# Kernel optimization log

Measured on AMD Instinct MI355X. Metric: run time of the kernel, lower is better.

## Reference

```python
import jax, jax.numpy as jnp
import numpy as np

EPS = 1e-6

def rms_norm(x):
    # RMSNorm, affine=False
    return x * jax.lax.rsqrt(jnp.mean(x * x, axis=-1, keepdims=True) + EPS)

def apply_rope(x, cos, sin):
    # x: [N, T, h, d], cos/sin: [T, d//2], half-split rotation
    x1, x2 = jnp.split(x, 2, axis=-1)
    c = cos[None, :, None, :]
    s = sin[None, :, None, :]
    return jnp.concatenate([x1 * c - x2 * s, x1 * s + x2 * c], axis=-1)

def setup_inputs() -> dict:
    key = jax.random.key(0)
    k0, k1, k2 = jax.random.split(key, 3)
    N, T, D, hd = 1, 2048, 2048, 128
    input_NTD = jax.random.normal(k0, (N, T, D), jnp.float32)
    qkv_weight = jax.random.normal(k1, (3, D, D), jnp.float32) / np.sqrt(D) / 2.0
    o_weight = jax.random.normal(k2, (D, D), jnp.float32) * 0.02
    # standard 1d RoPE angle table
    pos = jnp.arange(T, dtype=jnp.float32)
    inv_freq = 1.0 / (10000.0 ** (jnp.arange(hd // 2, dtype=jnp.float32) / (hd // 2)))
    ang = pos[:, None] * inv_freq[None, :]  # [T, hd//2]
    return {
        "input_NTD": input_NTD,
        "qkv_weight": qkv_weight,
        "o_weight": o_weight,
        "cos": jnp.cos(ang),
        "sin": jnp.sin(ang),
    }

def reference(input_NTD, qkv_weight, o_weight, cos, sin):
    N, T, D = input_NTD.shape
    hd = cos.shape[-1] * 2
    h = D // hd
    w = qkv_weight.reshape(3 * D, D)
    qkv = rms_norm(input_NTD) @ w.T                      # [N, T, 3D]
    qkv = qkv.reshape(N, T, 3 * h, hd)
    q, k, v = jnp.split(qkv, 3, axis=2)                  # each [N, T, h, hd]
    q = apply_rope(rms_norm(q), cos, sin)
    k = apply_rope(rms_norm(k), cos, sin)
    scale = 1.0 / np.sqrt(hd)
    scores = jnp.einsum('nqhd,nkhd->nhqk', q, k) * scale  # [N, h, T, T]
    causal = jnp.tril(jnp.ones((T, T), bool))
    scores = jnp.where(causal[None, None], scores, -jnp.inf)
    att = jax.nn.softmax(scores, axis=-1)
    x = jnp.einsum('nhqk,nkhd->nqhd', att, v).reshape(N, T, D)
    out = input_NTD + x @ o_weight.T
    return out, k, v
```

## Files before the change

kernel.cpp:

```cpp
#include <hip/hip_runtime.h>
#include <hip/hip_bf16.h>

typedef unsigned short u16;
typedef unsigned int u32;
typedef __bf16 bf16x8 __attribute__((ext_vector_type(8)));
typedef u16 u16x8 __attribute__((ext_vector_type(8)));
typedef u16 u16x4 __attribute__((ext_vector_type(4)));
typedef float f32x4 __attribute__((ext_vector_type(4)));

#define T_SEQ 2048
#define DMODEL 2048
#define NHEAD 16
#define HDIM 128
#define ATT_SCALE_L2E 0.12751744f

__device__ __forceinline__ u16 f2bf(float f) {
    return __builtin_bit_cast(u16, __float2bfloat16(f));
}
__device__ __forceinline__ bf16x8 as_bf(u16x8 v) {
    return __builtin_bit_cast(bf16x8, v);
}
__device__ __forceinline__ float lo2f(u32 w) { return __builtin_bit_cast(float, w << 16); }
__device__ __forceinline__ float hi2f(u32 w) { return __builtin_bit_cast(float, w & 0xffff0000u); }
__device__ __forceinline__ void gload_lds16(const u16* g, u16* l) {
    __builtin_amdgcn_global_load_lds(
        (const __attribute__((address_space(1))) u32*)(g),
        (__attribute__((address_space(3))) u32*)(l), 16, 0, 0);
}

__global__ __launch_bounds__(256) void cast_both(const float* __restrict__ w1,
                                                 const float* __restrict__ w2,
                                                 u16* __restrict__ d1,
                                                 u16* __restrict__ d2) {
    int i = blockIdx.x * 256 + threadIdx.x;
    const float* src; u16* dst; int k;
    if (i < 1572864) { src = w1; dst = d1; k = i; }
    else             { src = w2; dst = d2; k = i - 1572864; }
    float4 a = ((const float4*)src)[2 * k];
    float4 b = ((const float4*)src)[2 * k + 1];
    u16x8 o;
    o[0] = f2bf(a.x); o[1] = f2bf(a.y); o[2] = f2bf(a.z); o[3] = f2bf(a.w);
    o[4] = f2bf(b.x); o[5] = f2bf(b.y); o[6] = f2bf(b.z); o[7] = f2bf(b.w);
    *(u16x8*)(dst + (size_t)k * 8) = o;
}

__global__ __launch_bounds__(256) void rmsnorm_row(const float* __restrict__ x,
                                                   u16* __restrict__ xn) {
    const int row = blockIdx.x, tid = threadIdx.x;
    const float* xr = x + (size_t)row * DMODEL;
    float4 a = ((const float4*)xr)[2 * tid];
    float4 b = ((const float4*)xr)[2 * tid + 1];
    float ss = a.x*a.x + a.y*a.y + a.z*a.z + a.w*a.w
             + b.x*b.x + b.y*b.y + b.z*b.z + b.w*b.w;
#pragma unroll
    for (int off = 32; off; off >>= 1) ss += __shfl_xor(ss, off);
    __shared__ float red[4];
    if ((tid & 63) == 0) red[tid >> 6] = ss;
    __syncthreads();
    float tot = red[0] + red[1] + red[2] + red[3];
    float r = rsqrtf(tot * (1.f / DMODEL) + 1e-6f);
    u16x8 o;
    o[0] = f2bf(a.x*r); o[1] = f2bf(a.y*r); o[2] = f2bf(a.z*r); o[3] = f2bf(a.w*r);
    o[4] = f2bf(b.x*r); o[5] = f2bf(b.y*r); o[6] = f2bf(b.z*r); o[7] = f2bf(b.w*r);
    *(u16x8*)(xn + (size_t)row * DMODEL + tid * 8) = o;
}

#define VM2 asm volatile("s_waitcnt vmcnt(2)" ::: "memory");
#define VM4 asm volatile("s_waitcnt vmcnt(4)" ::: "memory");
#define VM0 asm volatile("s_waitcnt vmcnt(0)" ::: "memory");

#define ENDP                                                                  \
  __builtin_amdgcn_s_barrier();                                               \
  __builtin_amdgcn_sched_barrier(0);

#define LDA192(BUF, MH)                                                       \
  _Pragma("unroll") for (int mq = 0; mq < 4; ++mq) {                          \
    int ra = wr + (MH) * 64 + mq * 16 + fr;                                   \
    int sw = ra & 7;                                                          \
    _Pragma("unroll") for (int k2 = 0; k2 < 2; ++k2)                          \
      av[mq][k2] = *(const u16x8*)(sA[BUF] + ra * 64 +                        \
                                   ((((k2 << 2) | fg) ^ sw) << 3));           \
  }

#define LDB0_192(BUF)                                                         \
  _Pragma("unroll") for (int nq = 0; nq < 2; ++nq) {                          \
    int rb = wc + nq * 16 + fr;                                               \
    int sw = rb & 7;                                                          \
    _Pragma("unroll") for (int k2 = 0; k2 < 2; ++k2)                          \
      bv[nq][k2] = *(const u16x8*)(sB[BUF] + rb * 64 +                        \
                                   ((((k2 << 2) | fg) ^ sw) << 3));           \
  }

#define LDB1_192(BUF)                                                         \
  {                                                                           \
    int rb = wc + 32 + fr;                                                    \
    int sw = rb & 7;                                                          \
    _Pragma("unroll") for (int k2 = 0; k2 < 2; ++k2)                          \
      bv1[k2] = *(const u16x8*)(sB[BUF] + rb * 64 +                           \
                                ((((k2 << 2) | fg) ^ sw) << 3));              \
  }

#define MFMAQ_N0(MH)                                                          \
  __builtin_amdgcn_s_barrier();                                               \
  __builtin_amdgcn_s_setprio(1);                                              \
  _Pragma("unroll") for (int k2 = 0; k2 < 2; ++k2)                            \
    _Pragma("unroll") for (int mq = 0; mq < 4; ++mq)                          \
      _Pragma("unroll") for (int nq = 0; nq < 2; ++nq)                        \
        acc[(MH) * 4 + mq][nq] = __builtin_amdgcn_mfma_f32_16x16x32_bf16(     \
            as_bf(av[mq][k2]), as_bf(bv[nq][k2]), acc[(MH) * 4 + mq][nq],     \
            0, 0, 0);                                                         \
  __builtin_amdgcn_s_setprio(0);

#define MFMAQ_N1(MH)                                                          \
  __builtin_amdgcn_s_barrier();                                               \
  __builtin_amdgcn_s_setprio(1);                                              \
  _Pragma("unroll") for (int k2 = 0; k2 < 2; ++k2)                            \
    _Pragma("unroll") for (int mq = 0; mq < 4; ++mq)                          \
      acc[(MH) * 4 + mq][2] = __builtin_amdgcn_mfma_f32_16x16x32_bf16(        \
          as_bf(av[mq][k2]), as_bf(bv1[k2]), acc[(MH) * 4 + mq][2],           \
          0, 0, 0);                                                           \
  __builtin_amdgcn_s_setprio(0);

__global__ __launch_bounds__(512) void gemm192(const u16* __restrict__ A,
                                               const u16* __restrict__ B,
                                               u16* __restrict__ C,
                                               int M, int N, int K) {
    extern __shared__ char smem[];
    const int tid = threadIdx.x, lane = tid & 63, wid = tid >> 6;
    const int bm = blockIdx.y * 256, bn = blockIdx.x * 192;
    const int wr = (wid >> 2) * 128, wc = (wid & 3) * 48;
    const int fr = lane & 15, fg = lane >> 4;

    u16* sA[2] = {(u16*)smem, (u16*)(smem + 57344)};
    u16* sB[2] = {(u16*)(smem + 32768), (u16*)(smem + 90112)};

    const int cs = (((tid & 7) ^ ((tid >> 3) & 7)) << 3);
    const int s8 = (tid & 7) << 3;
    const int rr6 = tid >> 3;

    auto stA = [&](int buf, int k0, int mh) {
#pragma unroll
        for (int j = 0; j < 2; ++j) {
            int r = j * 128 + mh * 64 + rr6;
            gload_lds16(A + (size_t)(bm + r) * K + k0 + cs, sA[buf] + r * 64 + s8);
        }
    };
    auto stB = [&](int buf, int k0, int bt) {
        int r = bt * 64 + rr6;
        gload_lds16(B + (size_t)(bn + r) * K + k0 + cs, sB[buf] + r * 64 + s8);
    };

    f32x4 acc[8][3] = {};
    u16x8 av[4][2], bv[2][2], bv1[2];
    const int nt = K >> 6;

    stA(0, 0, 0); stA(0, 0, 1); stB(0, 0, 0); stB(0, 0, 1); stB(0, 0, 2);
    stA(1, 64, 0);
    VM2
    __builtin_amdgcn_s_barrier();
    __builtin_amdgcn_sched_barrier(0);

    for (int it = 0; it < (nt >> 1); ++it) {
        const int kc = it << 7;
        const int kn1 = kc + 64, kn2 = kc + 128, kn3 = kc + 192;
        const bool st2 = (kn2 < K), st3 = (kn3 < K);

        LDA192(0, 0) LDB0_192(0)
        stA(1, kn1, 1); stB(1, kn1, 0);
        MFMAQ_N0(0) ENDP
        LDB1_192(0)
        stB(1, kn1, 1); stB(1, kn1, 2);
        MFMAQ_N1(0) ENDP
        LDA192(0, 1)
        if (st2) stA(0, kn2, 0);
        MFMAQ_N1(1) ENDP
        LDB0_192(0)
        MFMAQ_N0(1)
        if (st2) { VM2 } else { VM0 }
        ENDP
        LDA192(1, 0) LDB0_192(1)
        if (st2) { stA(0, kn2, 1); stB(0, kn2, 0); }
        MFMAQ_N0(0) ENDP
        LDB1_192(1)
        if (st2) { stB(0, kn2, 1); stB(0, kn2, 2); }
        MFMAQ_N1(0) ENDP
        LDA192(1, 1)
        if (st3) stA(1, kn3, 0);
        MFMAQ_N1(1) ENDP
        LDB0_192(1)
        MFMAQ_N0(1)
        if (st3) { VM2 } else { VM0 }
        ENDP
    }

#pragma unroll
    for (int am = 0; am < 8; ++am)
#pragma unroll
        for (int bq = 0; bq < 3; ++bq)
#pragma unroll
            for (int r = 0; r < 4; ++r) {
                int row = bm + wr + am * 16 + fg * 4 + r;
                int col = bn + wc + bq * 16 + fr;
                C[(size_t)row * N + col] = f2bf(acc[am][bq][r]);
            }
}

#define LDAH(BUF, MH)                                                         \
  _Pragma("unroll") for (int mq = 0; mq < 2; ++mq) {                          \
    int ra = wr + (MH) * 32 + mq * 16 + fr;                                   \
    int sw = ra & 7;                                                          \
    _Pragma("unroll") for (int k2 = 0; k2 < 2; ++k2)                          \
      av[mq][k2] = *(const u16x8*)(sA[BUF] + ra * 64 +                        \
                                   ((((k2 << 2) | fg) ^ sw) << 3));           \
  }

#define LDBH(BUF, NH)                                                         \
  _Pragma("unroll") for (int nq = 0; nq < 2; ++nq) {                          \
    int rb = wc + (NH) * 32 + nq * 16 + fr;                                   \
    int sw = rb & 7;                                                          \
    _Pragma("unroll") for (int k2 = 0; k2 < 2; ++k2)                          \
      bv[nq][k2] = *(const u16x8*)(sB[BUF] + rb * 64 +                        \
                                   ((((k2 << 2) | fg) ^ sw) << 3));           \
  }

#define MFMAQH(MH, NH)                                                        \
  __builtin_amdgcn_s_barrier();                                               \
  __builtin_amdgcn_s_setprio(1);                                              \
  _Pragma("unroll") for (int k2 = 0; k2 < 2; ++k2)                            \
    _Pragma("unroll") for (int mq = 0; mq < 2; ++mq)                          \
      _Pragma("unroll") for (int nq = 0; nq < 2; ++nq)                        \
        acc[(MH) * 2 + mq][(NH) * 2 + nq] =                                   \
            __builtin_amdgcn_mfma_f32_16x16x32_bf16(                          \
                as_bf(av[mq][k2]), as_bf(bv[nq][k2]),                         \
                acc[(MH) * 2 + mq][(NH) * 2 + nq], 0, 0, 0);                  \
  __builtin_amdgcn_s_setprio(0);

__global__ __launch_bounds__(256) void gemm128(const u16* __restrict__ A,
                                               const u16* __restrict__ B,
                                               float* __restrict__ C,
                                               const float* __restrict__ resid,
                                               int M, int N, int K) {
    extern __shared__ char smem[];
    const int tid = threadIdx.x, lane = tid & 63, wid = tid >> 6;
    const int bm = blockIdx.y * 128, bn = blockIdx.x * 128;
    const int wr = (wid >> 1) * 64, wc = (wid & 1) * 64;
    const int fr = lane & 15, fg = lane >> 4;

    u16* sA[2] = {(u16*)smem, (u16*)(smem + 32768)};
    u16* sB[2] = {(u16*)(smem + 16384), (u16*)(smem + 49152)};

    const int cs = (((tid & 7) ^ ((tid >> 3) & 7)) << 3);
    const int s8 = (tid & 7) << 3;
    const int rr5 = tid >> 3;

    auto stA = [&](int buf, int k0, int mh) {
#pragma unroll
        for (int j = 0; j < 2; ++j) {
            int r = j * 64 + mh * 32 + rr5;
            gload_lds16(A + (size_t)(bm + r) * K + k0 + cs, sA[buf] + r * 64 + s8);
        }
    };
    auto stB = [&](int buf, int k0, int nh) {
#pragma unroll
        for (int j = 0; j < 2; ++j) {
            int r = j * 64 + nh * 32 + rr5;
            gload_lds16(B + (size_t)(bn + r) * K + k0 + cs, sB[buf] + r * 64 + s8);
        }
    };

    f32x4 acc[4][4] = {};
    u16x8 av[2][2], bv[2][2];
    const int nt = K >> 6;

    stA(0, 0, 0); stA(0, 0, 1); stB(0, 0, 0); stB(0, 0, 1);
    stA(1, 64, 0); stB(1, 64, 1);
    VM4
    __builtin_amdgcn_s_barrier();
    __builtin_amdgcn_sched_barrier(0);

    for (int it = 0; it < (nt >> 1); ++it) {
        const int kc = it << 7;
        const int kn1 = kc + 64, kn2 = kc + 128, kn3 = kc + 192;
        const bool st2 = (kn2 < K), st3 = (kn3 < K);

        LDAH(0, 0) LDBH(0, 0)
        stA(1, kn1, 1);
        MFMAQH(0, 0) ENDP
        LDBH(0, 1)
        stB(1, kn1, 0);
        MFMAQH(0, 1) ENDP
        LDAH(0, 1)
        if (st2) stA(0, kn2, 0);
        MFMAQH(1, 1) ENDP
        LDBH(0, 0)
        if (st2) stB(0, kn2, 1);
        MFMAQH(1, 0)
        if (st2) { VM4 } else { VM0 }
        ENDP
        LDAH(1, 0) LDBH(1, 0)
        if (st2) stA(0, kn2, 1);
        MFMAQH(0, 0) ENDP
        LDBH(1, 1)
        if (st2) stB(0, kn2, 0);
        MFMAQH(0, 1) ENDP
        LDAH(1, 1)
        if (st3) stA(1, kn3, 0);
        MFMAQH(1, 1) ENDP
        LDBH(1, 0)
        if (st3) stB(1, kn3, 1);
        MFMAQH(1, 0)
        VM4
        ENDP
    }

#pragma unroll
    for (int am = 0; am < 4; ++am)
#pragma unroll
        for (int bq = 0; bq < 4; ++bq)
#pragma unroll
            for (int r = 0; r < 4; ++r) {
                int row = bm + wr + am * 16 + fg * 4 + r;
                int col = bn + wc + bq * 16 + fr;
                float val = acc[am][bq][r] + resid[(size_t)row * N + col];
                C[(size_t)row * N + col] = val;
            }
}

__global__ __launch_bounds__(256) void rope_split(const u16* __restrict__ qkv,
                                                  const float* __restrict__ cosb,
                                                  const float* __restrict__ sinb,
                                                  u16* __restrict__ q_bf,
                                                  u16* __restrict__ k_bf,
                                                  float* __restrict__ k_out,
                                                  float* __restrict__ v_out) {
    const int t = blockIdx.x, tid = threadIdx.x, wid = tid >> 6, lane = tid & 63;
    const u16* row = qkv + (size_t)t * (3 * DMODEL);
    const int dp = (lane & 31) << 1;
    float2 c2 = *(const float2*)(cosb + t * 64 + dp);
    float2 s2 = *(const float2*)(sinb + t * 64 + dp);
    const bool hi = lane >= 32;

    for (int task = wid; task < 32; task += 4) {
        u32 w = *(const u32*)(row + task * 128 + lane * 2);
        float xa = lo2f(w), xb = hi2f(w);
        float ss = xa * xa + xb * xb;
#pragma unroll
        for (int off = 32; off; off >>= 1) ss += __shfl_xor(ss, off);
        float rn = rsqrtf(ss * (1.f / 128.f) + 1e-6f);
        float pa = __shfl_xor(xa, 32), pb = __shfl_xor(xb, 32);
        float oa, ob;
        if (!hi) {
            oa = (xa * c2.x - pa * s2.x) * rn;
            ob = (xb * c2.y - pb * s2.y) * rn;
        } else {
            oa = (pa * s2.x + xa * c2.x) * rn;
            ob = (pb * s2.y + xb * c2.y) * rn;
        }
        u32 pk = (u32)f2bf(oa) | ((u32)f2bf(ob) << 16);
        if (task < 16) {
            *(u32*)(q_bf + ((size_t)task * T_SEQ + t) * 128 + lane * 2) = pk;
        } else {
            int hh = task - 16;
            *(u32*)(k_bf + ((size_t)hh * T_SEQ + t) * 128 + lane * 2) = pk;
            float2 kk; kk.x = oa; kk.y = ob;
            *(float2*)(k_out + (size_t)t * DMODEL + hh * 128 + lane * 2) = kk;
        }
    }
    {
        u16x8 vv = *(const u16x8*)(row + 2 * DMODEL + tid * 8);
        float4 f0, f1;
        f0.x = __builtin_bit_cast(float, (u32)vv[0] << 16);
        f0.y = __builtin_bit_cast(float, (u32)vv[1] << 16);
        f0.z = __builtin_bit_cast(float, (u32)vv[2] << 16);
        f0.w = __builtin_bit_cast(float, (u32)vv[3] << 16);
        f1.x = __builtin_bit_cast(float, (u32)vv[4] << 16);
        f1.y = __builtin_bit_cast(float, (u32)vv[5] << 16);
        f1.z = __builtin_bit_cast(float, (u32)vv[6] << 16);
        f1.w = __builtin_bit_cast(float, (u32)vv[7] << 16);
        *(float4*)(v_out + (size_t)t * DMODEL + tid * 8) = f0;
        *(float4*)(v_out + (size_t)t * DMODEL + tid * 8 + 4) = f1;
    }
}

__global__ __launch_bounds__(256) void vtrans(const u16* __restrict__ qkv,
                                              u16* __restrict__ vt) {
    const int b = blockIdx.x, tid = threadIdx.x;
    const int head = b >> 7;
    const int i = (b & 127) * 256 + tid;
    const int d = i & 127, tc = i >> 7;
    u16x8 o;
#pragma unroll
    for (int j = 0; j < 8; ++j)
        o[j] = qkv[(size_t)(tc * 8 + j) * (3 * DMODEL) + 2 * DMODEL + head * 128 + d];
    *(u16x8*)&vt[((size_t)head * 128 + d) * T_SEQ + tc * 8] = o;
}

__global__ __launch_bounds__(256) void attn_fwd(const u16* __restrict__ qb,
                                                const u16* __restrict__ kb,
                                                const u16* __restrict__ vtb,
                                                u16* __restrict__ xout) {
    __shared__ u16 Ks[2][64 * 128];
    __shared__ u16 Vs[2][128 * 64];
    __shared__ u16 Ps[4][16 * 64];

    const int bid = blockIdx.x;
    const int r8 = bid & 7, s = bid >> 3;
    const int head = r8 + ((s >> 5) << 3);
    const int j = s & 31;
    const int qt = (s < 32) ? (31 - j) : j;

    const int tid = threadIdx.x, wid = tid >> 6, lane = tid & 63;
    const int fr = lane & 15, fg = lane >> 4;
    const u16* kh = kb + (size_t)head * T_SEQ * 128;
    const u16* vth = vtb + (size_t)head * 128 * T_SEQ;
    const u16* qh = qb + (size_t)head * T_SEQ * 128;
    const int q0 = qt * 64 + wid * 16;
    const int qrow_g = q0 + fr;

    u16x8 bq[4];
    {
        const u16* qrow = qh + (size_t)(q0 + fr) * 128 + fg * 8;
#pragma unroll
        for (int cc = 0; cc < 4; ++cc) bq[cc] = *(const u16x8*)(qrow + cc * 32);
    }

    auto stage = [&](int kv0, int buf) {
#pragma unroll
        for (int i = 0; i < 4; ++i) {
            int idx = i * 256 + tid;
            int r = idx >> 4;
            int cbs = ((idx & 15) << 4) ^ ((r & 7) << 4);
            gload_lds16(kh + (size_t)(kv0 + r) * 128 + (cbs >> 1), &Ks[buf][idx * 8]);
        }
#pragma unroll
        for (int i = 0; i < 4; ++i) {
            int idx = i * 256 + tid;
            int d = idx >> 3;
            int cbs = ((idx & 7) << 4) ^ ((d & 7) << 4);
            gload_lds16(vth + (size_t)d * T_SEQ + kv0 + (cbs >> 1), &Vs[buf][idx * 8]);
        }
    };

    stage(0, 0);

    f32x4 o[8] = {};
    float m_run = -1e30f, l_run = 0.f;
    const int nt = qt + 1;

    for (int kt = 0; kt < nt; ++kt) {
        const int kv0 = kt * 64;
        const int buf = kt & 1;
        if (kt + 1 < nt) {
            stage(kv0 + 64, buf ^ 1);
            asm volatile("s_waitcnt vmcnt(8)" ::: "memory");
        } else {
            asm volatile("s_waitcnt vmcnt(0)" ::: "memory");
        }
        __builtin_amdgcn_s_barrier();
        __builtin_amdgcn_sched_barrier(0);

        const char* ksb = (const char*)&Ks[buf][0];
        const char* vsb = (const char*)&Vs[buf][0];
        char* psb = (char*)&Ps[wid][0];

        float p[4][4];
        float mx = -1e30f;
        const bool diag = (kv0 + 64 > q0);
#pragma unroll
        for (int st = 0; st < 4; ++st) {
            f32x4 sacc = {0.f, 0.f, 0.f, 0.f};
#pragma unroll
            for (int c4 = 0; c4 < 4; ++c4) {
                int r = st * 16 + fr;
                int cb = c4 * 64 + fg * 16;
                u16x8 ak = *(const u16x8*)(ksb + r * 256 + (cb ^ ((r & 7) << 4)));
                sacc = __builtin_amdgcn_mfma_f32_16x16x32_bf16(
                    as_bf(ak), as_bf(bq[c4]), sacc, 0, 0, 0);
            }
#pragma unroll
            for (int rr = 0; rr < 4; ++rr) {
                float sv = sacc[rr] * ATT_SCALE_L2E;
                if (diag) {
                    int kvg = kv0 + st * 16 + fg * 4 + rr;
                    sv = (kvg <= qrow_g) ? sv : -1e30f;
                }
                p[st][rr] = sv;
                mx = fmaxf(mx, sv);
            }
        }
        mx = fmaxf(mx, __shfl_xor(mx, 16));
        mx = fmaxf(mx, __shfl_xor(mx, 32));

        if (__all(mx - m_run <= 11.5f)) {
            float rs = 0.f;
#pragma unroll
            for (int st = 0; st < 4; ++st) {
                u16x4 pw;
#pragma unroll
                for (int rr = 0; rr < 4; ++rr) {
                    float e = exp2f(p[st][rr] - m_run);
                    rs += e;
                    pw[rr] = f2bf(e);
                }
                *(u16x4*)(psb + fr * 128 + ((st * 32 + fg * 8) ^ ((fr & 7) << 4))) = pw;
            }
            rs += __shfl_xor(rs, 16);
            rs += __shfl_xor(rs, 32);
            l_run += rs;
        } else {
            float m_new = fmaxf(m_run, mx);
            float corr = exp2f(m_run - m_new);
            float rs = 0.f;
#pragma unroll
            for (int st = 0; st < 4; ++st) {
                u16x4 pw;
#pragma unroll
                for (int rr = 0; rr < 4; ++rr) {
                    float e = exp2f(p[st][rr] - m_new);
                    rs += e;
                    pw[rr] = f2bf(e);
                }
                *(u16x4*)(psb + fr * 128 + ((st * 32 + fg * 8) ^ ((fr & 7) << 4))) = pw;
            }
            rs += __shfl_xor(rs, 16);
            rs += __shfl_xor(rs, 32);
            l_run = l_run * corr + rs;
            m_run = m_new;
            float ct[4];
#pragma unroll
            for (int rr = 0; rr < 4; ++rr) ct[rr] = __shfl(corr, fg * 4 + rr);
#pragma unroll
            for (int f = 0; f < 8; ++f)
#pragma unroll
                for (int rr = 0; rr < 4; ++rr) o[f][rr] *= ct[rr];
        }

#pragma unroll
        for (int ks = 0; ks < 2; ++ks) {
            u16x8 pa = *(const u16x8*)(psb + fr * 128 + ((ks * 64 + fg * 16) ^ ((fr & 7) << 4)));
#pragma unroll
            for (int f = 0; f < 8; ++f) {
                int d = f * 16 + fr;
                u16x8 vB = *(const u16x8*)(vsb + d * 128 + ((ks * 64 + fg * 16) ^ ((d & 7) << 4)));
                o[f] = __builtin_amdgcn_mfma_f32_16x16x32_bf16(
                    as_bf(pa), as_bf(vB), o[f], 0, 0, 0);
            }
        }
        __builtin_amdgcn_s_barrier();
    }

    float li[4];
#pragma unroll
    for (int rr = 0; rr < 4; ++rr) li[rr] = __shfl(l_run, fg * 4 + rr);
#pragma unroll
    for (int f = 0; f < 8; ++f)
#pragma unroll
        for (int rr = 0; rr < 4; ++rr) {
            int trow = q0 + fg * 4 + rr;
            float val = o[f][rr] / li[rr];
            xout[(size_t)trow * DMODEL + head * 128 + f * 16 + fr] = f2bf(val);
        }
}

extern "C" void kernel_launch(void* const* d_in, const int* in_sizes, int n_in,
                              void* d_out, int out_size, void* d_ws, size_t ws_size,
                              hipStream_t stream) {
    const float* x_in = (const float*)d_in[0];
    const float* w_qkv = (const float*)d_in[1];
    const float* w_o = (const float*)d_in[2];
    const float* cosb = (const float*)d_in[3];
    const float* sinb = (const float*)d_in[4];

    float* out = (float*)d_out;
    float* k_out = out + 4194304;
    float* v_out = out + 8388608;

    char* ws = (char*)d_ws;
    u16* xn    = (u16*)(ws);
    u16* w_bf  = (u16*)(ws + (size_t)(8u << 20));
    u16* o_bf  = (u16*)(ws + (size_t)(32u << 20));
    u16* qkv   = (u16*)(ws + (size_t)(40u << 20));
    u16* q_bf  = (u16*)(ws + (size_t)(64u << 20));
    u16* k_bf  = (u16*)(ws + (size_t)(72u << 20));
    u16* vt_bf = (u16*)(ws + (size_t)(80u << 20));
    u16* x_bf  = (u16*)(ws + (size_t)(88u << 20));

    (void)hipFuncSetAttribute(reinterpret_cast<const void*>(&gemm192),
                              hipFuncAttributeMaxDynamicSharedMemorySize, 114688);
    (void)hipFuncSetAttribute(reinterpret_cast<const void*>(&gemm128),
                              hipFuncAttributeMaxDynamicSharedMemorySize, 65536);

    cast_both<<<8192, 256, 0, stream>>>(w_qkv, w_o, w_bf, o_bf);
    rmsnorm_row<<<2048, 256, 0, stream>>>(x_in, xn);
    gemm192<<<dim3(32, 8), 512, 114688, stream>>>(xn, w_bf, qkv, 2048, 6144, 2048);
    rope_split<<<2048, 256, 0, stream>>>(qkv, cosb, sinb, q_bf, k_bf, k_out, v_out);
    vtrans<<<2048, 256, 0, stream>>>(qkv, vt_bf);
    attn_fwd<<<512, 256, 0, stream>>>(q_bf, k_bf, vt_bf, x_bf);
    gemm128<<<dim3(16, 16), 256, 65536, stream>>>(x_bf, o_bf, out, x_in, 2048, 2048, 2048);
}
```

Before: 185.4 us.

## Merge weight cast and RMSNorm into one launch; switch softmax to natural exp

Combines the bf16 weight-cast kernel and the input RMSNorm kernel into a single prep kernel with a block-index split, removing one launch and its gap. The attention softmax now scales scores by 1/sqrt(d) and uses __expf instead of folding log2(e) into the scale and using exp2f, with the lazy-rescale threshold changed to 8. __expf is typically implemented as a multiply by log2(e) followed by exp2, so this adds an extra multiply per element and may trigger more rescales.

```diff
diff --git a/kernel.cpp b/kernel.cpp
--- a/kernel.cpp
+++ b/kernel.cpp
@@ -12,7 +12,7 @@
 #define DMODEL 2048
 #define NHEAD 16
 #define HDIM 128
-#define ATT_SCALE_L2E 0.12751744f
+#define ATT_SCALE 0.08838834764831843f
 
 __device__ __forceinline__ u16 f2bf(float f) {
     return __builtin_bit_cast(u16, __float2bfloat16(f));
@@ -28,30 +28,32 @@
         (__attribute__((address_space(3))) u32*)(l), 16, 0, 0);
 }
 
-__global__ __launch_bounds__(256) void cast_both(const float* __restrict__ w1,
-                                                 const float* __restrict__ w2,
-                                                 u16* __restrict__ d1,
-                                                 u16* __restrict__ d2) {
-    int i = blockIdx.x * 256 + threadIdx.x;
-    const float* src; u16* dst; int k;
-    if (i < 1572864) { src = w1; dst = d1; k = i; }
-    else             { src = w2; dst = d2; k = i - 1572864; }
-    float4 a = ((const float4*)src)[2 * k];
-    float4 b = ((const float4*)src)[2 * k + 1];
-    u16x8 o;
-    o[0] = f2bf(a.x); o[1] = f2bf(a.y); o[2] = f2bf(a.z); o[3] = f2bf(a.w);
-    o[4] = f2bf(b.x); o[5] = f2bf(b.y); o[6] = f2bf(b.z); o[7] = f2bf(b.w);
-    *(u16x8*)(dst + (size_t)k * 8) = o;
-}
-
-__global__ __launch_bounds__(256) void rmsnorm_row(const float* __restrict__ x,
-                                                   u16* __restrict__ xn) {
-    const int row = blockIdx.x, tid = threadIdx.x;
+__global__ __launch_bounds__(256) void prep(const float* __restrict__ w1,
+                                            const float* __restrict__ w2,
+                                            const float* __restrict__ x,
+                                            u16* __restrict__ d1,
+                                            u16* __restrict__ d2,
+                                            u16* __restrict__ xn) {
+    const int b = blockIdx.x, tid = threadIdx.x;
+    if (b < 8192) {
+        int i = b * 256 + tid;
+        const float* src; u16* dst; int k;
+        if (i < 1572864) { src = w1; dst = d1; k = i; }
+        else             { src = w2; dst = d2; k = i - 1572864; }
+        float4 a = ((const float4*)src)[2 * k];
+        float4 bb = ((const float4*)src)[2 * k + 1];
+        u16x8 o;
+        o[0] = f2bf(a.x); o[1] = f2bf(a.y); o[2] = f2bf(a.z); o[3] = f2bf(a.w);
+        o[4] = f2bf(bb.x); o[5] = f2bf(bb.y); o[6] = f2bf(bb.z); o[7] = f2bf(bb.w);
+        *(u16x8*)(dst + (size_t)k * 8) = o;
+        return;
+    }
+    const int row = b - 8192;
     const float* xr = x + (size_t)row * DMODEL;
     float4 a = ((const float4*)xr)[2 * tid];
-    float4 b = ((const float4*)xr)[2 * tid + 1];
+    float4 bb = ((const float4*)xr)[2 * tid + 1];
     float ss = a.x*a.x + a.y*a.y + a.z*a.z + a.w*a.w
-             + b.x*b.x + b.y*b.y + b.z*b.z + b.w*b.w;
+             + bb.x*bb.x + bb.y*bb.y + bb.z*bb.z + bb.w*bb.w;
 #pragma unroll
     for (int off = 32; off; off >>= 1) ss += __shfl_xor(ss, off);
     __shared__ float red[4];
@@ -61,7 +63,7 @@
     float r = rsqrtf(tot * (1.f / DMODEL) + 1e-6f);
     u16x8 o;
     o[0] = f2bf(a.x*r); o[1] = f2bf(a.y*r); o[2] = f2bf(a.z*r); o[3] = f2bf(a.w*r);
-    o[4] = f2bf(b.x*r); o[5] = f2bf(b.y*r); o[6] = f2bf(b.z*r); o[7] = f2bf(b.w*r);
+    o[4] = f2bf(bb.x*r); o[5] = f2bf(bb.y*r); o[6] = f2bf(bb.z*r); o[7] = f2bf(bb.w*r);
     *(u16x8*)(xn + (size_t)row * DMODEL + tid * 8) = o;
 }
 
@@ -479,7 +481,7 @@
             }
 #pragma unroll
             for (int rr = 0; rr < 4; ++rr) {
-                float sv = sacc[rr] * ATT_SCALE_L2E;
+                float sv = sacc[rr] * ATT_SCALE;
                 if (diag) {
                     int kvg = kv0 + st * 16 + fg * 4 + rr;
                     sv = (kvg <= qrow_g) ? sv : -1e30f;
@@ -491,14 +493,14 @@
         mx = fmaxf(mx, __shfl_xor(mx, 16));
         mx = fmaxf(mx, __shfl_xor(mx, 32));
 
-        if (__all(mx - m_run <= 11.5f)) {
+        if (__all(mx - m_run <= 8.f)) {
             float rs = 0.f;
 #pragma unroll
             for (int st = 0; st < 4; ++st) {
                 u16x4 pw;
 #pragma unroll
                 for (int rr = 0; rr < 4; ++rr) {
-                    float e = exp2f(p[st][rr] - m_run);
+                    float e = __expf(p[st][rr] - m_run);
                     rs += e;
                     pw[rr] = f2bf(e);
                 }
@@ -509,14 +511,14 @@
             l_run += rs;
         } else {
             float m_new = fmaxf(m_run, mx);
-            float corr = exp2f(m_run - m_new);
+            float corr = __expf(m_run - m_new);
             float rs = 0.f;
 #pragma unroll
             for (int st = 0; st < 4; ++st) {
                 u16x4 pw;
 #pragma unroll
                 for (int rr = 0; rr < 4; ++rr) {
-                    float e = exp2f(p[st][rr] - m_new);
+                    float e = __expf(p[st][rr] - m_new);
                     rs += e;
                     pw[rr] = f2bf(e);
                 }
@@ -590,8 +592,7 @@
     (void)hipFuncSetAttribute(reinterpret_cast<const void*>(&gemm128),
                               hipFuncAttributeMaxDynamicSharedMemorySize, 65536);
 
-    cast_both<<<8192, 256, 0, stream>>>(w_qkv, w_o, w_bf, o_bf);
-    rmsnorm_row<<<2048, 256, 0, stream>>>(x_in, xn);
+    prep<<<10240, 256, 0, stream>>>(w_qkv, w_o, x_in, w_bf, o_bf, xn);
     gemm192<<<dim3(32, 8), 512, 114688, stream>>>(xn, w_bf, qkv, 2048, 6144, 2048);
     rope_split<<<2048, 256, 0, stream>>>(qkv, cosb, sinb, q_bf, k_bf, k_out, v_out);
     vtrans<<<2048, 256, 0, stream>>>(qkv, vt_bf);
```

New measurement: 179.3 us. 3.3% less time.
